# Performance work log

Measured on AMD Instinct MI355X. Metric: run time of the kernel, lower is better.

Reference implementation:

```python
import jax, jax.numpy as jnp
import numpy as np

# KroneckerLinear: W ~= sum_i (A_i kron B_i); efficient path computes, per token,
# Y = sum_i A_i @ X @ B_i^T with X = x.reshape(in1, in2), output flattened as (out1*out2).

IN1, IN2 = 64, 64      # in_factors (in1*in2 = in_features = 4096)
OUT1, OUT2 = 64, 64    # out_factors (out1*out2 = out_features = 4096)
NUM_SUM = 2
BATCH, SEQ = 4, 4096


def setup_inputs() -> dict:
    key = jax.random.key(0)
    kx, ka, kb, kbias = jax.random.split(key, 4)
    x = jax.random.normal(kx, (BATCH, SEQ, IN1 * IN2), dtype=jnp.float32)
    # kaiming-uniform-like scale for small factors
    bound_a = 1.0 / np.sqrt(IN1)
    bound_b = 1.0 / np.sqrt(IN2)
    A = jax.random.uniform(ka, (NUM_SUM, OUT1, IN1), dtype=jnp.float32, minval=-bound_a, maxval=bound_a)
    B = jax.random.uniform(kb, (NUM_SUM, OUT2, IN2), dtype=jnp.float32, minval=-bound_b, maxval=bound_b)
    bound = 1.0 / np.sqrt(IN1 * IN2)
    bias = jax.random.uniform(kbias, (OUT1 * OUT2,), dtype=jnp.float32, minval=-bound, maxval=bound)
    return {"x": x, "A": A, "B": B, "bias": bias}


def reference(x, A, B, bias):
    Bsz, T, _ = x.shape
    X = x.reshape(Bsz, T, IN1, IN2)  # (b, t, i, j)
    # y[b,t,o,p] = sum_s sum_ij A[s,o,i] * X[b,t,i,j] * B[s,p,j]  -> (out1, out2)
    y = jnp.einsum("btij,soi,spj->btop", X, A, B)
    return y.reshape(Bsz, T, OUT1 * OUT2) + bias
```

## Files before the change

kernel.cpp:

```cpp
#include <hip/hip_runtime.h>
#include <hip/hip_bf16.h>

typedef float  f32x4  __attribute__((ext_vector_type(4)));
typedef short  bf16x8 __attribute__((ext_vector_type(8)));

#define NT      16384
#define NBLOCK  256
#define TPS     (NT / NBLOCK)

__device__ __forceinline__ short f2bf(float x) {
  return (short)__builtin_bit_cast(unsigned short, __float2bfloat16(x));
}
__device__ __forceinline__ unsigned packbf2(float a, float b) {
  return (unsigned)(unsigned short)f2bf(a) | ((unsigned)(unsigned short)f2bf(b) << 16);
}

__device__ __forceinline__ void gload16(const float* gp, float* lp) {
  __builtin_amdgcn_global_load_lds((const __attribute__((address_space(1))) void*)gp,
                                   (__attribute__((address_space(3))) void*)lp,
                                   16, 0, 0);
}
__device__ __forceinline__ unsigned ldsaddr(const void* p) {
  return (unsigned)(uintptr_t)(const __attribute__((address_space(3))) void*)p;
}

__device__ __forceinline__ void stageQW(float* XB, const float* gbase, int j, int lane) {
#pragma unroll
  for (int qq = 0; qq < 4; ++qq) {
    const int q = j * 4 + qq;
    const int i = q * 4 + (lane >> 4);
    const float* gp = gbase + i * 64 + (((lane & 15) ^ (i & 7)) << 2);
    gload16(gp, XB + q * 256);
  }
}

__global__ __launch_bounds__(512, 1)
void kron_kernel(const float* __restrict__ x,
                 const float* __restrict__ A,
                 const float* __restrict__ Bm,
                 const float* __restrict__ bias,
                 float* __restrict__ out) {
  __shared__ float  xb[4][4096];
  __shared__ bf16x8 AT[1024];
  __shared__ bf16x8 BT[1024];
  __shared__ unsigned long long Ul[2048];

  const int tid  = threadIdx.x;
  const int lane = tid & 63;
  const int w    = tid >> 6;
  const int j    = w & 3;
  const int g    = lane >> 4;
  const int l15  = lane & 15;
  const int blk  = blockIdx.x;
  const bool consumer = (w < 4);

  f32x4 bv[4];
  if (consumer) {
#pragma unroll
    for (int t = 0; t < 4; ++t) {
      const int idx = j * 4 + t;
      const int s = idx >> 3, ot = (idx & 7) >> 1, c = idx & 1;
      const int o = ot * 16 + l15;
      bf16x8 v;
#pragma unroll
      for (int e = 0; e < 8; ++e) {
        const int i = c * 32 + 4 * g + (e & 3) + 16 * (e >> 2);
        v[e] = f2bf(A[s * 4096 + o * 64 + i]);
      }
      AT[idx * 64 + lane] = v;
    }
#pragma unroll
    for (int t = 0; t < 4; ++t) {
      const int idx = j * 4 + t;
      const int s = idx >> 3, pt = (idx & 7) >> 1, jc = idx & 1;
      const int p = pt * 16 + l15;
      bf16x8 v;
#pragma unroll
      for (int e = 0; e < 8; ++e)
        v[e] = f2bf(Bm[s * 4096 + p * 64 + (jc * 32 + 8 * g + e)]);
      BT[idx * 64 + lane] = v;
    }
#pragma unroll
    for (int ot = 0; ot < 4; ++ot)
      bv[ot] = *(const f32x4*)(bias + (ot * 16 + l15) * 64 + j * 16 + 4 * g);
  }
  __syncthreads();

  if (!consumer) {
    stageQW(&xb[0][0], x + ((size_t)blk << 12),                j, lane);
    stageQW(&xb[1][0], x + ((size_t)(blk + NBLOCK) << 12),     j, lane);
    stageQW(&xb[2][0], x + ((size_t)(blk + 2 * NBLOCK) << 12), j, lane);
    asm volatile("s_waitcnt vmcnt(8)" ::: "memory");
  }
  __builtin_amdgcn_s_barrier();

  const unsigned wsw = (unsigned)(2 * ((l15 >> 2) & 1));

  for (int k = 0; k < TPS; ++k) {
    if (consumer) {
      const unsigned ba   = ldsaddr(&xb[k & 3][0]);
      const unsigned base = ba + (unsigned)(j * 16 + l15) * 256u;
      const unsigned m    = (unsigned)(l15 & 7);
      f32x4 r0[2], r1[2];
#pragma unroll
      for (int jc = 0; jc < 2; ++jc) {
        const unsigned c0 = (unsigned)(8 * jc + 2 * g);
        asm volatile("ds_read_b128 %0, %1" : "=v"(r0[jc]) : "v"(base + ((c0 ^ m) << 4)) : "memory");
        asm volatile("ds_read_b128 %0, %1" : "=v"(r1[jc]) : "v"(base + (((c0 + 1u) ^ m) << 4)) : "memory");
      }
      asm volatile("s_waitcnt lgkmcnt(0)" ::: "memory");
      __builtin_amdgcn_sched_barrier(0);

      bf16x8 xf[2];
#pragma unroll
      for (int jc = 0; jc < 2; ++jc) {
        bf16x8 t;
        t[0]=f2bf(r0[jc][0]); t[1]=f2bf(r0[jc][1]); t[2]=f2bf(r0[jc][2]); t[3]=f2bf(r0[jc][3]);
        t[4]=f2bf(r1[jc][0]); t[5]=f2bf(r1[jc][1]); t[6]=f2bf(r1[jc][2]); t[7]=f2bf(r1[jc][3]);
        xf[jc] = t;
      }

#pragma unroll
      for (int s = 0; s < 2; ++s) {
#pragma unroll
        for (int pt = 0; pt < 4; ++pt) {
          f32x4 a1 = (f32x4){0.f, 0.f, 0.f, 0.f};
#pragma unroll
          for (int jc = 0; jc < 2; ++jc)
            a1 = __builtin_amdgcn_mfma_f32_16x16x32_bf16(
                xf[jc], BT[(s * 8 + pt * 2 + jc) * 64 + lane], a1, 0, 0, 0);
          const unsigned lo = packbf2(a1[0], a1[1]);
          const unsigned hi = packbf2(a1[2], a1[3]);
          Ul[((((s * 4 + pt) * 4 + g) * 16 + l15) << 2) + ((unsigned)j ^ wsw)] =
              ((unsigned long long)hi << 32) | lo;
        }
      }
      asm volatile("s_waitcnt lgkmcnt(0)" ::: "memory");
      __builtin_amdgcn_sched_barrier(0);
    } else {
      if (k + 3 < TPS)
        stageQW(&xb[(k + 3) & 3][0],
                x + ((size_t)(blk + (k + 3) * NBLOCK) << 12), j, lane);
    }

    __builtin_amdgcn_s_barrier();

    if (consumer) {
      f32x4 acc[4];
#pragma unroll
      for (int ot = 0; ot < 4; ++ot) acc[ot] = bv[ot];
#pragma unroll
      for (int s = 0; s < 2; ++s) {
        bf16x8 uf[2];
#pragma unroll
        for (int c = 0; c < 2; ++c) {
          const unsigned q2 = (unsigned)((l15 >> 2) & 1);
          uf[c] = *reinterpret_cast<const bf16x8*>(
              &Ul[((((s * 4 + j) * 4 + g) * 16 + l15) << 2) + 2u * ((unsigned)c ^ q2)]);
        }
#pragma unroll
        for (int ot = 0; ot < 4; ++ot)
#pragma unroll
          for (int c = 0; c < 2; ++c)
            acc[ot] = __builtin_amdgcn_mfma_f32_16x16x32_bf16(
                uf[c], AT[(s * 8 + ot * 2 + c) * 64 + lane], acc[ot], 0, 0, 0);
      }
      float* ob = out + ((size_t)(blk + k * NBLOCK) << 12);
#pragma unroll
      for (int ot = 0; ot < 4; ++ot)
        *(f32x4*)(ob + (ot * 16 + l15) * 64 + j * 16 + 4 * g) = acc[ot];
    } else {
      if (k < TPS - 3)       asm volatile("s_waitcnt vmcnt(8)" ::: "memory");
      else if (k == TPS - 3) asm volatile("s_waitcnt vmcnt(4)" ::: "memory");
      else                   asm volatile("s_waitcnt vmcnt(0)" ::: "memory");
    }

    __builtin_amdgcn_s_barrier();
  }
}

extern "C" void kernel_launch(void* const* d_in, const int* in_sizes, int n_in,
                              void* d_out, int out_size, void* d_ws, size_t ws_size,
                              hipStream_t stream) {
  const float* x    = (const float*)d_in[0];
  const float* A    = (const float*)d_in[1];
  const float* B    = (const float*)d_in[2];
  const float* bias = (const float*)d_in[3];
  float* out        = (float*)d_out;
  kron_kernel<<<dim3(NBLOCK), dim3(512), 0, stream>>>(x, A, B, bias, out);
}
```

Before: 100.5 us.

## Software-pipeline the two GEMM stages with double-buffered U and one barrier per token

Double-buffers the intermediate U in LDS so stage 2 for token k-1 runs in the same phase as stage 1 for token k. This halves the block barriers per iteration and overlaps the LDS reads of X with the stage-2 MFMAs. The producer prefetch depth drops from three tokens ahead to two, which reduces memory-latency hiding. There is also a possible hazard: the xb buffer being refilled may still be read if the barrier ordering is off.

```diff
diff --git a/kernel.cpp b/kernel.cpp
--- a/kernel.cpp
+++ b/kernel.cpp
@@ -43,7 +43,7 @@
   __shared__ float  xb[4][4096];
   __shared__ bf16x8 AT[1024];
   __shared__ bf16x8 BT[1024];
-  __shared__ unsigned long long Ul[2048];
+  __shared__ unsigned long long Ul[2][2048];
 
   const int tid  = threadIdx.x;
   const int lane = tid & 63;
@@ -87,95 +87,96 @@
   __syncthreads();
 
   if (!consumer) {
-    stageQW(&xb[0][0], x + ((size_t)blk << 12),                j, lane);
-    stageQW(&xb[1][0], x + ((size_t)(blk + NBLOCK) << 12),     j, lane);
-    stageQW(&xb[2][0], x + ((size_t)(blk + 2 * NBLOCK) << 12), j, lane);
-    asm volatile("s_waitcnt vmcnt(8)" ::: "memory");
+    stageQW(&xb[0][0], x + ((size_t)blk << 12),            j, lane);
+    stageQW(&xb[1][0], x + ((size_t)(blk + NBLOCK) << 12), j, lane);
+    asm volatile("s_waitcnt vmcnt(4)" ::: "memory");
   }
   __builtin_amdgcn_s_barrier();
 
   const unsigned wsw = (unsigned)(2 * ((l15 >> 2) & 1));
+  const unsigned q2  = (unsigned)((l15 >> 2) & 1);
 
-  for (int k = 0; k < TPS; ++k) {
+  for (int k = 0; k <= TPS; ++k) {
     if (consumer) {
-      const unsigned ba   = ldsaddr(&xb[k & 3][0]);
-      const unsigned base = ba + (unsigned)(j * 16 + l15) * 256u;
-      const unsigned m    = (unsigned)(l15 & 7);
       f32x4 r0[2], r1[2];
+      if (k < TPS) {
+        const unsigned ba   = ldsaddr(&xb[k & 3][0]);
+        const unsigned base = ba + (unsigned)(j * 16 + l15) * 256u;
+        const unsigned m    = (unsigned)(l15 & 7);
 #pragma unroll
-      for (int jc = 0; jc < 2; ++jc) {
-        const unsigned c0 = (unsigned)(8 * jc + 2 * g);
-        asm volatile("ds_read_b128 %0, %1" : "=v"(r0[jc]) : "v"(base + ((c0 ^ m) << 4)) : "memory");
-        asm volatile("ds_read_b128 %0, %1" : "=v"(r1[jc]) : "v"(base + (((c0 + 1u) ^ m) << 4)) : "memory");
-      }
-      asm volatile("s_waitcnt lgkmcnt(0)" ::: "memory");
-      __builtin_amdgcn_sched_barrier(0);
-
-      bf16x8 xf[2];
-#pragma unroll
-      for (int jc = 0; jc < 2; ++jc) {
-        bf16x8 t;
-        t[0]=f2bf(r0[jc][0]); t[1]=f2bf(r0[jc][1]); t[2]=f2bf(r0[jc][2]); t[3]=f2bf(r0[jc][3]);
-        t[4]=f2bf(r1[jc][0]); t[5]=f2bf(r1[jc][1]); t[6]=f2bf(r1[jc][2]); t[7]=f2bf(r1[jc][3]);
-        xf[jc] = t;
+        for (int jc = 0; jc < 2; ++jc) {
+          const unsigned c0 = (unsigned)(8 * jc + 2 * g);
+          asm volatile("ds_read_b128 %0, %1" : "=v"(r0[jc]) : "v"(base + ((c0 ^ m) << 4)) : "memory");
+          asm volatile("ds_read_b128 %0, %1" : "=v"(r1[jc]) : "v"(base + (((c0 + 1u) ^ m) << 4)) : "memory");
+        }
       }
 
+      if (k > 0) {
+        const unsigned long long* Up = &Ul[(k - 1) & 1][0];
+        f32x4 acc[4];
 #pragma unroll
-      for (int s = 0; s < 2; ++s) {
+        for (int ot = 0; ot < 4; ++ot) acc[ot] = bv[ot];
 #pragma unroll
-        for (int pt = 0; pt < 4; ++pt) {
-          f32x4 a1 = (f32x4){0.f, 0.f, 0.f, 0.f};
+        for (int s = 0; s < 2; ++s) {
+          bf16x8 uf[2];
 #pragma unroll
-          for (int jc = 0; jc < 2; ++jc)
-            a1 = __builtin_amdgcn_mfma_f32_16x16x32_bf16(
-                xf[jc], BT[(s * 8 + pt * 2 + jc) * 64 + lane], a1, 0, 0, 0);
-          const unsigned lo = packbf2(a1[0], a1[1]);
-          const unsigned hi = packbf2(a1[2], a1[3]);
-          Ul[((((s * 4 + pt) * 4 + g) * 16 + l15) << 2) + ((unsigned)j ^ wsw)] =
-              ((unsigned long long)hi << 32) | lo;
+          for (int c = 0; c < 2; ++c)
+            uf[c] = *reinterpret_cast<const bf16x8*>(
+                &Up[((((s * 4 + j) * 4 + g) * 16 + l15) << 2) + 2u * ((unsigned)c ^ q2)]);
+#pragma unroll
+          for (int ot = 0; ot < 4; ++ot)
+#pragma unroll
+            for (int c = 0; c < 2; ++c)
+              acc[ot] = __builtin_amdgcn_mfma_f32_16x16x32_bf16(
+                  uf[c], AT[(s * 8 + ot * 2 + c) * 64 + lane], acc[ot], 0, 0, 0);
         }
+        float* ob = out + ((size_t)(blk + (k - 1) * NBLOCK) << 12);
+#pragma unroll
+        for (int ot = 0; ot < 4; ++ot)
+          *(f32x4*)(ob + (ot * 16 + l15) * 64 + j * 16 + 4 * g) = acc[ot];
       }
-      asm volatile("s_waitcnt lgkmcnt(0)" ::: "memory");
-      __builtin_amdgcn_sched_barrier(0);
+
+      if (k < TPS) {
+        asm volatile("s_waitcnt lgkmcnt(0)" ::: "memory");
+        __builtin_amdgcn_sched_barrier(0);
+        bf16x8 xf[2];
+#pragma unroll
+        for (int jc = 0; jc < 2; ++jc) {
+          bf16x8 t;
+          t[0]=f2bf(r0[jc][0]); t[1]=f2bf(r0[jc][1]); t[2]=f2bf(r0[jc][2]); t[3]=f2bf(r0[jc][3]);
+          t[4]=f2bf(r1[jc][0]); t[5]=f2bf(r1[jc][1]); t[6]=f2bf(r1[jc][2]); t[7]=f2bf(r1[jc][3]);
+          xf[jc] = t;
+        }
+        unsigned long long* Uw = &Ul[k & 1][0];
+#pragma unroll
+        for (int s = 0; s < 2; ++s) {
+#pragma unroll
+          for (int pt = 0; pt < 4; ++pt) {
+            f32x4 a1 = (f32x4){0.f, 0.f, 0.f, 0.f};
+#pragma unroll
+            for (int jc = 0; jc < 2; ++jc)
+              a1 = __builtin_amdgcn_mfma_f32_16x16x32_bf16(
+                  xf[jc], BT[(s * 8 + pt * 2 + jc) * 64 + lane], a1, 0, 0, 0);
+            const unsigned lo = packbf2(a1[0], a1[1]);
+            const unsigned hi = packbf2(a1[2], a1[3]);
+            Uw[((((s * 4 + pt) * 4 + g) * 16 + l15) << 2) + ((unsigned)j ^ wsw)] =
+                ((unsigned long long)hi << 32) | lo;
+          }
+        }
+        asm volatile("s_waitcnt lgkmcnt(0)" ::: "memory");
+        __builtin_amdgcn_sched_barrier(0);
+      }
     } else {
-      if (k + 3 < TPS)
-        stageQW(&xb[(k + 3) & 3][0],
-                x + ((size_t)(blk + (k + 3) * NBLOCK) << 12), j, lane);
+      if (k + 2 < TPS) {
+        stageQW(&xb[(k + 2) & 3][0],
+                x + ((size_t)(blk + (k + 2) * NBLOCK) << 12), j, lane);
+        asm volatile("s_waitcnt vmcnt(4)" ::: "memory");
+      } else {
+        asm volatile("s_waitcnt vmcnt(0)" ::: "memory");
+      }
     }
 
-    __builtin_amdgcn_s_barrier();
-
-    if (consumer) {
-      f32x4 acc[4];
-#pragma unroll
-      for (int ot = 0; ot < 4; ++ot) acc[ot] = bv[ot];
-#pragma unroll
-      for (int s = 0; s < 2; ++s) {
-        bf16x8 uf[2];
-#pragma unroll
-        for (int c = 0; c < 2; ++c) {
-          const unsigned q2 = (unsigned)((l15 >> 2) & 1);
-          uf[c] = *reinterpret_cast<const bf16x8*>(
-              &Ul[((((s * 4 + j) * 4 + g) * 16 + l15) << 2) + 2u * ((unsigned)c ^ q2)]);
-        }
-#pragma unroll
-        for (int ot = 0; ot < 4; ++ot)
-#pragma unroll
-          for (int c = 0; c < 2; ++c)
-            acc[ot] = __builtin_amdgcn_mfma_f32_16x16x32_bf16(
-                uf[c], AT[(s * 8 + ot * 2 + c) * 64 + lane], acc[ot], 0, 0, 0);
-      }
-      float* ob = out + ((size_t)(blk + k * NBLOCK) << 12);
-#pragma unroll
-      for (int ot = 0; ot < 4; ++ot)
-        *(f32x4*)(ob + (ot * 16 + l15) * 64 + j * 16 + 4 * g) = acc[ot];
-    } else {
-      if (k < TPS - 3)       asm volatile("s_waitcnt vmcnt(8)" ::: "memory");
-      else if (k == TPS - 3) asm volatile("s_waitcnt vmcnt(4)" ::: "memory");
-      else                   asm volatile("s_waitcnt vmcnt(0)" ::: "memory");
-    }
-
-    __builtin_amdgcn_s_barrier();
+    if (k < TPS) __builtin_amdgcn_s_barrier();
   }
 }
 
```

Measured after the change: 112.6 us. 12.0% more time.
